# Kernel optimization log

Hardware: AMD Instinct MI355X
Metric: run time of the kernel (lower is better)

## Reference

```python
import jax, jax.numpy as jnp
import numpy as np

OVERSAMP = 2


def _pad_last2(x, H2, W2):
    # centered zero-pad of last two dims to (H2, W2) -- PadLast
    H, W = x.shape[-2], x.shape[-1]
    ph, pw = (H2 - H) // 2, (W2 - W) // 2
    pad = [(0, 0)] * (x.ndim - 2) + [(ph, H2 - H - ph), (pw, W2 - W - pw)]
    return jnp.pad(x, pad)


def _crop_last2(x, H, W):
    # centered crop of last two dims to (H, W) -- PadLast.adjoint
    H2, W2 = x.shape[-2], x.shape[-1]
    ph, pw = (H2 - H) // 2, (W2 - W) // 2
    return x[..., ph:ph + H, pw:pw + W]


def setup_inputs() -> dict:
    key = jax.random.key(0)
    ks = jax.random.split(key, 6)
    A, C, H, W = 5, 12, 256, 256
    Hp, Wp = OVERSAMP * H, OVERSAMP * W
    x_r = jax.random.normal(ks[0], (A, H, W), dtype=jnp.float32)
    x_i = jax.random.normal(ks[1], (A, H, W), dtype=jnp.float32)
    mps_r = jax.random.normal(ks[2], (C, H, W), dtype=jnp.float32) * 0.1
    mps_i = jax.random.normal(ks[3], (C, H, W), dtype=jnp.float32) * 0.1
    kern_r = jax.random.normal(ks[4], (A, A, Hp, Wp), dtype=jnp.float32) * 0.1
    kern_i = jax.random.normal(ks[5], (A, A, Hp, Wp), dtype=jnp.float32) * 0.1
    return {"x_r": x_r, "x_i": x_i, "mps_r": mps_r, "mps_i": mps_i,
            "kern_r": kern_r, "kern_i": kern_i}


def reference(x_r, x_i, mps_r, mps_i, kern_r, kern_i):
    # Toeplitz normal operator AHA_func: x [A,H,W] -> [A,H,W]
    x = jax.lax.complex(x_r, x_i)          # [A,H,W]
    mps = jax.lax.complex(mps_r, mps_i)    # [C,H,W]
    kernels = jax.lax.complex(kern_r, kern_i)  # [Aout,Ain,2H,2W]
    A, H, W = x.shape
    Hp, Wp = kernels.shape[-2], kernels.shape[-1]
    # coil modulation: x[None,:] * mps[:,None] -> [C,A,H,W]
    cx = mps[:, None, :, :] * x[None, :, :, :]
    cx = _pad_last2(cx, Hp, Wp)            # [C,A,2H,2W]
    Fx = jnp.fft.fftn(cx, axes=(-2, -1), norm='ortho')
    # Fx[:,None] [C,1,Ain,2H,2W] * kernels [Aout,Ain,2H,2W] -> [C,Aout,Ain,2H,2W]
    y = (OVERSAMP ** 2) * jnp.fft.ifftn(Fx[:, None, ...] * kernels,
                                        axes=(-2, -1), norm='ortho')
    y = jnp.sum(y, axis=2)                 # sum over Ain -> [C,Aout,2H,2W]
    y = _crop_last2(y, H, W)               # [C,A,H,W]
    y = y * jnp.conj(mps)[:, None, :, :]
    return jnp.sum(y, axis=0)              # [A,H,W]
```

## Files before the change

kernel.cpp:

```cpp
#include <hip/hip_runtime.h>
#include <cstddef>

#define PI_F 3.14159265358979323846f
#define A_  5
#define C_  12
#define RPG (C_ * A_)

__device__ float2 g_bufA[RPG * 256 * 512];
__device__ float2 g_bufB[RPG * 512 * 256];
__device__ float2 g_xT[5  * 65536];
__device__ float2 g_mT[12 * 65536];
__device__ float2 g_oT[5  * 65536];

#define NP 528
__device__ inline int PADI(int i) { return i + (i >> 5); }
__device__ inline int PADT(int i) { return i + (i >> 3); }

__device__ inline void build_tabP(float2* tab, int t) {
    #pragma unroll
    for (int q = 0; q < 2; ++q) {
        int k = t + q * 128;
        float s, c;
        __sincosf(-2.0f * PI_F * (float)k * (1.0f / 512.0f), &s, &c);
        tab[PADT(k)] = make_float2(c, s);
    }
}

template<int DIR>
__device__ inline float2 cmulw(float2 v, float2 w) {
    float cv = w.x, sv = (DIR < 0) ? w.y : -w.y;
    return make_float2(v.x * cv - v.y * sv, v.x * sv + v.y * cv);
}

template<int DIR>
__device__ void fft512(float* Ar, float* Ai, float* Br, float* Bi,
                       const float2* tab, int t) {
    float *srcR = Ar, *srcI = Ai, *dstR = Br, *dstI = Bi;
    int Ns = 1;
    #pragma unroll
    for (int s = 0; s < 4; ++s) {
        __syncthreads();
        int j = t;
        int m = j & (Ns - 1);
        int e1 = m << (7 - 2 * s);
        float2 w1 = tab[PADT(e1)], w2 = tab[PADT(2 * e1)];
        float2 w3 = make_float2(w1.x * w2.x - w1.y * w2.y,
                                w1.x * w2.y + w1.y * w2.x);
        int i0 = PADI(j), i1 = PADI(j + 128), i2 = PADI(j + 256), i3 = PADI(j + 384);
        float2 v0 = make_float2(srcR[i0], srcI[i0]);
        float2 v1 = cmulw<DIR>(make_float2(srcR[i1], srcI[i1]), w1);
        float2 v2 = cmulw<DIR>(make_float2(srcR[i2], srcI[i2]), w2);
        float2 v3 = cmulw<DIR>(make_float2(srcR[i3], srcI[i3]), w3);
        float2 t0 = make_float2(v0.x + v2.x, v0.y + v2.y);
        float2 t1 = make_float2(v0.x - v2.x, v0.y - v2.y);
        float2 t2 = make_float2(v1.x + v3.x, v1.y + v3.y);
        float2 t3 = make_float2(v1.x - v3.x, v1.y - v3.y);
        float2 y0 = make_float2(t0.x + t2.x, t0.y + t2.y);
        float2 y2 = make_float2(t0.x - t2.x, t0.y - t2.y);
        float2 y1, y3;
        if (DIR < 0) {
            y1 = make_float2(t1.x + t3.y, t1.y - t3.x);
            y3 = make_float2(t1.x - t3.y, t1.y + t3.x);
        } else {
            y1 = make_float2(t1.x - t3.y, t1.y + t3.x);
            y3 = make_float2(t1.x + t3.y, t1.y - t3.x);
        }
        int idxD = ((j & ~(Ns - 1)) << 2) | m;
        int o0 = PADI(idxD), o1 = PADI(idxD + Ns);
        int o2 = PADI(idxD + 2 * Ns), o3 = PADI(idxD + 3 * Ns);
        dstR[o0] = y0.x; dstI[o0] = y0.y;
        dstR[o1] = y1.x; dstI[o1] = y1.y;
        dstR[o2] = y2.x; dstI[o2] = y2.y;
        dstR[o3] = y3.x; dstI[o3] = y3.y;
        float* tr = srcR; srcR = dstR; dstR = tr;
        float* ti = srcI; srcI = dstI; dstI = ti;
        Ns <<= 2;
    }
    __syncthreads();
    #pragma unroll
    for (int q = 0; q < 2; ++q) {
        int j = t + q * 128;
        float2 w = tab[PADT(j)];
        int i0 = PADI(j), i1 = PADI(j + 256);
        float2 v0 = make_float2(srcR[i0], srcI[i0]);
        float2 tw = cmulw<DIR>(make_float2(srcR[i1], srcI[i1]), w);
        dstR[i0] = v0.x + tw.x; dstI[i0] = v0.y + tw.y;
        dstR[i1] = v0.x - tw.x; dstI[i1] = v0.y - tw.y;
    }
    __syncthreads();
}

__global__ void k_inT(const float* __restrict__ xr, const float* __restrict__ xi,
                      const float* __restrict__ mr, const float* __restrict__ mi) {
    __shared__ float tR[32][33], tI[32][33];
    int z = blockIdx.z;
    const float* pr; const float* pi; float2* dst;
    if (z < 5) {
        pr = xr + (size_t)z * 65536; pi = xi + (size_t)z * 65536;
        dst = g_xT + (size_t)z * 65536;
    } else {
        int c = z - 5;
        pr = mr + (size_t)c * 65536; pi = mi + (size_t)c * 65536;
        dst = g_mT + (size_t)c * 65536;
    }
    int w0 = blockIdx.x * 32, h0 = blockIdx.y * 32;
    int tx = threadIdx.x, ty = threadIdx.y;
    for (int i = ty; i < 32; i += 8) {
        size_t idx = (size_t)(h0 + i) * 256 + (w0 + tx);
        tR[i][tx] = pr[idx];
        tI[i][tx] = pi[idx];
    }
    __syncthreads();
    for (int i = ty; i < 32; i += 8)
        dst[(size_t)(w0 + i) * 256 + (h0 + tx)] =
            make_float2(tR[tx][i], tI[tx][i]);
}

__global__ void k_fft1c() {
    int row = blockIdx.x;
    int ca = row >> 8;
    int xcol = row & 255;
    int coil = ca / A_;
    int a = ca - coil * A_;
    int t = threadIdx.x;
    __shared__ float Are[NP], Aim[NP], Bre[NP], Bim[NP];
    __shared__ float2 tab[288];
    build_tabP(tab, t);
    const float2* xs = g_xT + (size_t)a * 65536 + (size_t)xcol * 256;
    const float2* ms = g_mT + (size_t)coil * 65536 + (size_t)xcol * 256;
    Are[PADI(t)] = 0.f;       Aim[PADI(t)] = 0.f;
    Are[PADI(t + 384)] = 0.f; Aim[PADI(t + 384)] = 0.f;
    {
        float2 xv = xs[t], mv = ms[t];
        int p = PADI(t + 128);
        Are[p] = xv.x * mv.x - xv.y * mv.y;
        Aim[p] = xv.x * mv.y + xv.y * mv.x;
        xv = xs[t + 128]; mv = ms[t + 128];
        p = PADI(t + 256);
        Are[p] = xv.x * mv.x - xv.y * mv.y;
        Aim[p] = xv.x * mv.y + xv.y * mv.x;
    }
    fft512<-1>(Are, Aim, Bre, Bim, tab, t);
    float2* o = (float2*)g_bufA + (size_t)row * 512;
    #pragma unroll
    for (int q = 0; q < 4; ++q) {
        int k = t + q * 128;
        int p = PADI(k);
        o[k] = make_float2(Bre[p], Bim[p]);
    }
}

__global__ void __launch_bounds__(128) k_colfmc(const float* __restrict__ kr,
                                                const float* __restrict__ ki) {
    int b = blockIdx.x;
    int xcd = b & 7;
    int s = b >> 3;
    int v = s / 96, w = s % 96;
    int u = xcd + (v << 3);
    int coil = w % C_;
    int ky = (u << 3) + (w / C_);
    int t = threadIdx.x;
    __shared__ float Sre[NP], Sim[NP];
    __shared__ float FR[A_][NP], FI[A_][NP];
    __shared__ float2 tab[288];
    build_tabP(tab, t);

    for (int ain = 0; ain < A_; ++ain) {
        const float2* src = (const float2*)g_bufA +
                            ((size_t)(coil * A_ + ain) << 17);
        float2 v1 = src[(size_t)t * 512 + ky];
        float2 v2 = src[(size_t)(t + 128) * 512 + ky];
        Sre[PADI(t)] = 0.f;       Sim[PADI(t)] = 0.f;
        Sre[PADI(t + 384)] = 0.f; Sim[PADI(t + 384)] = 0.f;
        int p = PADI(t + 128);
        Sre[p] = v1.x; Sim[p] = v1.y;
        p = PADI(t + 256);
        Sre[p] = v2.x; Sim[p] = v2.y;
        fft512<-1>(Sre, Sim, FR[ain], FI[ain], tab, t);
    }

    const float scale = 4.0f / 262144.0f;
    size_t kyBase = (size_t)ky << 9;
    #pragma unroll
    for (int q = 0; q < 4; ++q) {
        int kx = t + q * 128;
        float krB[25], kiB[25];
        #pragma unroll
        for (int m = 0; m < 25; ++m) {
            size_t idx = ((size_t)m << 18) + kyBase + kx;
            krB[m] = kr[idx];
            kiB[m] = ki[idx];
        }
        int p = PADI(kx);
        float fr[A_], fi[A_];
        #pragma unroll
        for (int ain = 0; ain < A_; ++ain) {
            fr[ain] = FR[ain][p];
            fi[ain] = FI[ain][p];
        }
        #pragma unroll
        for (int aout = 0; aout < A_; ++aout) {
            float gr = 0.f, gi = 0.f;
            #pragma unroll
            for (int ain = 0; ain < A_; ++ain) {
                float kre = krB[aout * A_ + ain], kim = kiB[aout * A_ + ain];
                gr += kre * fr[ain] - kim * fi[ain];
                gi += kre * fi[ain] + kim * fr[ain];
            }
            FR[aout][p] = scale * gr;
            FI[aout][p] = scale * gi;
        }
    }

    for (int aout = 0; aout < A_; ++aout) {
        fft512<1>(FR[aout], FI[aout], Sre, Sim, tab, t);
        float4* o4 = (float4*)((float2*)g_bufB +
            ((size_t)(coil * A_ + aout) * 512 + ky) * 256);
        int x0 = 128 + 2 * t;
        int p0 = PADI(x0), p1 = PADI(x0 + 1);
        o4[t] = make_float4(Sre[p0], Sim[p0], Sre[p1], Sim[p1]);
    }
}

__global__ void k_outfr() {
    int b = blockIdx.x;
    int xcd = b & 7;
    int s = b >> 3;
    int v = s >> 3, w = s & 7;
    int g = xcd + (v << 3);
    int a = g >> 5;
    int xcol = ((g & 31) << 3) + w;
    int t = threadIdx.x;
    __shared__ float Are[NP], Aim[NP], Bre[NP], Bim[NP];
    __shared__ float2 tab[288];
    build_tabP(tab, t);
    float ar0 = 0.f, ai0 = 0.f, ar1 = 0.f, ai1 = 0.f;
    int y0 = 128 + 2 * t;
    for (int c = 0; c < C_; ++c) {
        const float2* src = (const float2*)g_bufB +
                            ((size_t)(c * A_ + a) << 17);
        #pragma unroll
        for (int q = 0; q < 4; ++q) {
            int kyq = t + q * 128;
            float2 vv = src[(size_t)kyq * 256 + xcol];
            int p = PADI(kyq);
            Are[p] = vv.x; Aim[p] = vv.y;
        }
        fft512<1>(Are, Aim, Bre, Bim, tab, t);
        const float4* mp4 = (const float4*)(g_mT + (size_t)c * 65536 +
                                            (size_t)xcol * 256);
        float4 mm = mp4[t];
        int p0 = PADI(y0), p1 = PADI(y0 + 1);
        float v0x = Bre[p0], v0y = Bim[p0];
        float v1x = Bre[p1], v1y = Bim[p1];
        ar0 += v0x * mm.x + v0y * mm.y;  ai0 += v0y * mm.x - v0x * mm.y;
        ar1 += v1x * mm.z + v1y * mm.w;  ai1 += v1y * mm.z - v1x * mm.w;
    }
    float4* o4 = (float4*)(g_oT + (size_t)a * 65536 + (size_t)xcol * 256);
    o4[t] = make_float4(ar0, ai0, ar1, ai1);
}

__global__ void k_outT(float* __restrict__ out, int outFloats) {
    __shared__ float tR[32][33], tI[32][33];
    int a = blockIdx.z;
    int x0 = blockIdx.x * 32, y0 = blockIdx.y * 32;
    const float2* src = g_oT + (size_t)a * 65536;
    int tx = threadIdx.x, ty = threadIdx.y;
    for (int i = ty; i < 32; i += 8) {
        float2 vv = src[(size_t)(x0 + i) * 256 + (y0 + tx)];
        tR[i][tx] = vv.x; tI[i][tx] = vv.y;
    }
    __syncthreads();
    for (int i = ty; i < 32; i += 8) {
        size_t reIdx = (size_t)a * 65536 + (size_t)(y0 + i) * 256 + (x0 + tx);
        size_t imIdx = 327680 + reIdx;
        if (reIdx < (size_t)outFloats) out[reIdx] = tR[tx][i];
        if (imIdx < (size_t)outFloats) out[imIdx] = tI[tx][i];
    }
}

extern "C" void kernel_launch(void* const* d_in, const int* in_sizes, int n_in,
                              void* d_out, int out_size, void* d_ws, size_t ws_size,
                              hipStream_t stream) {
    const float* xr = (const float*)d_in[0];
    const float* xi = (const float*)d_in[1];
    const float* mr = (const float*)d_in[2];
    const float* mi = (const float*)d_in[3];
    const float* kr = (const float*)d_in[4];
    const float* ki = (const float*)d_in[5];
    float* out = (float*)d_out;
    (void)d_ws; (void)ws_size; (void)n_in; (void)in_sizes;

    k_inT   <<<dim3(8, 8, 17), dim3(32, 8), 0, stream>>>(xr, xi, mr, mi);
    k_fft1c <<<RPG * 256, 128, 0, stream>>>();
    k_colfmc<<<C_ * 512, 128, 0, stream>>>(kr, ki);
    k_outfr <<<A_ * 256, 128, 0, stream>>>();
    k_outT  <<<dim3(8, 8, 5), dim3(32, 8), 0, stream>>>(out, out_size);
}
```

Baseline: 312.6 us.

## Transpose intermediate buffer layouts, prefetch next slices, and fuse final output transpose

Both intermediate spectra buffers are re-laid out so the column-FFT kernel and the output kernel read contiguous float4 rows, while the producing kernels now do strided scatter writes. The final transpose kernel and its staging buffer are removed: k_outfr writes the cropped, coil-combined result directly into the output with strided stores. Software prefetching of the next input slice is added to the ain and coil loops, the LDS padding scheme becomes i+(i>>3), and the XCD-aware block remapping in k_outfr is dropped. The net effect depends on whether coalesced reads outweigh the newly uncoalesced writes.

```diff
diff --git a/kernel.cpp b/kernel.cpp
--- a/kernel.cpp
+++ b/kernel.cpp
@@ -6,23 +6,21 @@
 #define C_  12
 #define RPG (C_ * A_)
 
-__device__ float2 g_bufA[RPG * 256 * 512];
-__device__ float2 g_bufB[RPG * 512 * 256];
+__device__ float2 g_bufA[RPG * 512 * 256];
+__device__ float2 g_bufB[RPG * 256 * 512];
 __device__ float2 g_xT[5  * 65536];
 __device__ float2 g_mT[12 * 65536];
-__device__ float2 g_oT[5  * 65536];
-
-#define NP 528
-__device__ inline int PADI(int i) { return i + (i >> 5); }
-__device__ inline int PADT(int i) { return i + (i >> 3); }
-
-__device__ inline void build_tabP(float2* tab, int t) {
+
+#define NP 576
+__device__ inline int P(int i) { return i + (i >> 3); }
+
+__device__ inline void build_tab(float2* tab, int t) {
     #pragma unroll
     for (int q = 0; q < 2; ++q) {
         int k = t + q * 128;
         float s, c;
         __sincosf(-2.0f * PI_F * (float)k * (1.0f / 512.0f), &s, &c);
-        tab[PADT(k)] = make_float2(c, s);
+        tab[P(k)] = make_float2(c, s);
     }
 }
 
@@ -43,10 +41,10 @@
         int j = t;
         int m = j & (Ns - 1);
         int e1 = m << (7 - 2 * s);
-        float2 w1 = tab[PADT(e1)], w2 = tab[PADT(2 * e1)];
+        float2 w1 = tab[P(e1)], w2 = tab[P(2 * e1)];
         float2 w3 = make_float2(w1.x * w2.x - w1.y * w2.y,
                                 w1.x * w2.y + w1.y * w2.x);
-        int i0 = PADI(j), i1 = PADI(j + 128), i2 = PADI(j + 256), i3 = PADI(j + 384);
+        int i0 = P(j), i1 = P(j + 128), i2 = P(j + 256), i3 = P(j + 384);
         float2 v0 = make_float2(srcR[i0], srcI[i0]);
         float2 v1 = cmulw<DIR>(make_float2(srcR[i1], srcI[i1]), w1);
         float2 v2 = cmulw<DIR>(make_float2(srcR[i2], srcI[i2]), w2);
@@ -66,8 +64,8 @@
             y3 = make_float2(t1.x + t3.y, t1.y - t3.x);
         }
         int idxD = ((j & ~(Ns - 1)) << 2) | m;
-        int o0 = PADI(idxD), o1 = PADI(idxD + Ns);
-        int o2 = PADI(idxD + 2 * Ns), o3 = PADI(idxD + 3 * Ns);
+        int o0 = P(idxD), o1 = P(idxD + Ns);
+        int o2 = P(idxD + 2 * Ns), o3 = P(idxD + 3 * Ns);
         dstR[o0] = y0.x; dstI[o0] = y0.y;
         dstR[o1] = y1.x; dstI[o1] = y1.y;
         dstR[o2] = y2.x; dstI[o2] = y2.y;
@@ -80,8 +78,8 @@
     #pragma unroll
     for (int q = 0; q < 2; ++q) {
         int j = t + q * 128;
-        float2 w = tab[PADT(j)];
-        int i0 = PADI(j), i1 = PADI(j + 256);
+        float2 w = tab[P(j)];
+        int i0 = P(j), i1 = P(j + 256);
         float2 v0 = make_float2(srcR[i0], srcI[i0]);
         float2 tw = cmulw<DIR>(make_float2(srcR[i1], srcI[i1]), w);
         dstR[i0] = v0.x + tw.x; dstI[i0] = v0.y + tw.y;
@@ -125,28 +123,25 @@
     int t = threadIdx.x;
     __shared__ float Are[NP], Aim[NP], Bre[NP], Bim[NP];
     __shared__ float2 tab[288];
-    build_tabP(tab, t);
-    const float2* xs = g_xT + (size_t)a * 65536 + (size_t)xcol * 256;
-    const float2* ms = g_mT + (size_t)coil * 65536 + (size_t)xcol * 256;
-    Are[PADI(t)] = 0.f;       Aim[PADI(t)] = 0.f;
-    Are[PADI(t + 384)] = 0.f; Aim[PADI(t + 384)] = 0.f;
-    {
-        float2 xv = xs[t], mv = ms[t];
-        int p = PADI(t + 128);
-        Are[p] = xv.x * mv.x - xv.y * mv.y;
-        Aim[p] = xv.x * mv.y + xv.y * mv.x;
-        xv = xs[t + 128]; mv = ms[t + 128];
-        p = PADI(t + 256);
-        Are[p] = xv.x * mv.x - xv.y * mv.y;
-        Aim[p] = xv.x * mv.y + xv.y * mv.x;
-    }
+    build_tab(tab, t);
+    const float4* xs4 = (const float4*)(g_xT + (size_t)a * 65536 + (size_t)xcol * 256);
+    const float4* ms4 = (const float4*)(g_mT + (size_t)coil * 65536 + (size_t)xcol * 256);
+    float4 xv = xs4[t], mv = ms4[t];
+    Are[P(t)] = 0.f;       Aim[P(t)] = 0.f;
+    Are[P(t + 384)] = 0.f; Aim[P(t + 384)] = 0.f;
+    int p = P(128 + 2 * t);
+    Are[p] = xv.x * mv.x - xv.y * mv.y;
+    Aim[p] = xv.x * mv.y + xv.y * mv.x;
+    p = P(129 + 2 * t);
+    Are[p] = xv.z * mv.z - xv.w * mv.w;
+    Aim[p] = xv.z * mv.w + xv.w * mv.z;
     fft512<-1>(Are, Aim, Bre, Bim, tab, t);
-    float2* o = (float2*)g_bufA + (size_t)row * 512;
+    float2* o = g_bufA + (size_t)ca * 131072 + xcol;
     #pragma unroll
     for (int q = 0; q < 4; ++q) {
-        int k = t + q * 128;
-        int p = PADI(k);
-        o[k] = make_float2(Bre[p], Bim[p]);
+        int ky = t + q * 128;
+        int pp = P(ky);
+        o[(size_t)ky * 256] = make_float2(Bre[pp], Bim[pp]);
     }
 }
 
@@ -163,20 +158,22 @@
     __shared__ float Sre[NP], Sim[NP];
     __shared__ float FR[A_][NP], FI[A_][NP];
     __shared__ float2 tab[288];
-    build_tabP(tab, t);
-
+    build_tab(tab, t);
+
+    const float2* bA = g_bufA + ((size_t)coil * A_) * 131072 + (size_t)ky * 256;
+    float4 cur = ((const float4*)bA)[t];
     for (int ain = 0; ain < A_; ++ain) {
-        const float2* src = (const float2*)g_bufA +
-                            ((size_t)(coil * A_ + ain) << 17);
-        float2 v1 = src[(size_t)t * 512 + ky];
-        float2 v2 = src[(size_t)(t + 128) * 512 + ky];
-        Sre[PADI(t)] = 0.f;       Sim[PADI(t)] = 0.f;
-        Sre[PADI(t + 384)] = 0.f; Sim[PADI(t + 384)] = 0.f;
-        int p = PADI(t + 128);
-        Sre[p] = v1.x; Sim[p] = v1.y;
-        p = PADI(t + 256);
-        Sre[p] = v2.x; Sim[p] = v2.y;
+        float4 nxt = cur;
+        if (ain + 1 < A_)
+            nxt = ((const float4*)(bA + (size_t)(ain + 1) * 131072))[t];
+        Sre[P(t)] = 0.f;       Sim[P(t)] = 0.f;
+        Sre[P(t + 384)] = 0.f; Sim[P(t + 384)] = 0.f;
+        int p = P(128 + 2 * t);
+        Sre[p] = cur.x; Sim[p] = cur.y;
+        p = P(129 + 2 * t);
+        Sre[p] = cur.z; Sim[p] = cur.w;
         fft512<-1>(Sre, Sim, FR[ain], FI[ain], tab, t);
+        cur = nxt;
     }
 
     const float scale = 4.0f / 262144.0f;
@@ -191,7 +188,7 @@
             krB[m] = kr[idx];
             kiB[m] = ki[idx];
         }
-        int p = PADI(kx);
+        int p = P(kx);
         float fr[A_], fi[A_];
         #pragma unroll
         for (int ain = 0; ain < A_; ++ain) {
@@ -214,69 +211,54 @@
 
     for (int aout = 0; aout < A_; ++aout) {
         fft512<1>(FR[aout], FI[aout], Sre, Sim, tab, t);
-        float4* o4 = (float4*)((float2*)g_bufB +
-            ((size_t)(coil * A_ + aout) * 512 + ky) * 256);
-        int x0 = 128 + 2 * t;
-        int p0 = PADI(x0), p1 = PADI(x0 + 1);
-        o4[t] = make_float4(Sre[p0], Sim[p0], Sre[p1], Sim[p1]);
-    }
-}
-
-__global__ void k_outfr() {
+        float2* oB = g_bufB + ((size_t)(coil * A_ + aout)) * 131072 + ky;
+        int p0 = P(128 + 2 * t), p1 = P(129 + 2 * t);
+        oB[(size_t)(2 * t) * 512]     = make_float2(Sre[p0], Sim[p0]);
+        oB[(size_t)(2 * t + 1) * 512] = make_float2(Sre[p1], Sim[p1]);
+    }
+}
+
+__global__ void k_outfr(float* __restrict__ out, int outFloats) {
     int b = blockIdx.x;
-    int xcd = b & 7;
-    int s = b >> 3;
-    int v = s >> 3, w = s & 7;
-    int g = xcd + (v << 3);
-    int a = g >> 5;
-    int xcol = ((g & 31) << 3) + w;
+    int a = b >> 8;
+    int xcol = b & 255;
     int t = threadIdx.x;
     __shared__ float Are[NP], Aim[NP], Bre[NP], Bim[NP];
     __shared__ float2 tab[288];
-    build_tabP(tab, t);
+    build_tab(tab, t);
     float ar0 = 0.f, ai0 = 0.f, ar1 = 0.f, ai1 = 0.f;
-    int y0 = 128 + 2 * t;
+    const float2* bB = g_bufB + (size_t)a * 131072 + (size_t)xcol * 512;
+    const float2* mT = g_mT + (size_t)xcol * 256;
+    float4 c0 = ((const float4*)bB)[t];
+    float4 c1 = ((const float4*)bB)[t + 128];
+    float4 cm = ((const float4*)mT)[t];
     for (int c = 0; c < C_; ++c) {
-        const float2* src = (const float2*)g_bufB +
-                            ((size_t)(c * A_ + a) << 17);
-        #pragma unroll
-        for (int q = 0; q < 4; ++q) {
-            int kyq = t + q * 128;
-            float2 vv = src[(size_t)kyq * 256 + xcol];
-            int p = PADI(kyq);
-            Are[p] = vv.x; Aim[p] = vv.y;
+        int p = P(2 * t);       Are[p] = c0.x; Aim[p] = c0.y;
+        p = P(2 * t + 1);       Are[p] = c0.z; Aim[p] = c0.w;
+        p = P(256 + 2 * t);     Are[p] = c1.x; Aim[p] = c1.y;
+        p = P(257 + 2 * t);     Are[p] = c1.z; Aim[p] = c1.w;
+        float4 n0 = c0, n1 = c1, nm = cm;
+        if (c + 1 < C_) {
+            const float2* nB = bB + (size_t)(c + 1) * A_ * 131072;
+            n0 = ((const float4*)nB)[t];
+            n1 = ((const float4*)nB)[t + 128];
+            nm = ((const float4*)(mT + (size_t)(c + 1) * 65536))[t];
         }
         fft512<1>(Are, Aim, Bre, Bim, tab, t);
-        const float4* mp4 = (const float4*)(g_mT + (size_t)c * 65536 +
-                                            (size_t)xcol * 256);
-        float4 mm = mp4[t];
-        int p0 = PADI(y0), p1 = PADI(y0 + 1);
+        int p0 = P(128 + 2 * t), p1 = P(129 + 2 * t);
         float v0x = Bre[p0], v0y = Bim[p0];
         float v1x = Bre[p1], v1y = Bim[p1];
-        ar0 += v0x * mm.x + v0y * mm.y;  ai0 += v0y * mm.x - v0x * mm.y;
-        ar1 += v1x * mm.z + v1y * mm.w;  ai1 += v1y * mm.z - v1x * mm.w;
-    }
-    float4* o4 = (float4*)(g_oT + (size_t)a * 65536 + (size_t)xcol * 256);
-    o4[t] = make_float4(ar0, ai0, ar1, ai1);
-}
-
-__global__ void k_outT(float* __restrict__ out, int outFloats) {
-    __shared__ float tR[32][33], tI[32][33];
-    int a = blockIdx.z;
-    int x0 = blockIdx.x * 32, y0 = blockIdx.y * 32;
-    const float2* src = g_oT + (size_t)a * 65536;
-    int tx = threadIdx.x, ty = threadIdx.y;
-    for (int i = ty; i < 32; i += 8) {
-        float2 vv = src[(size_t)(x0 + i) * 256 + (y0 + tx)];
-        tR[i][tx] = vv.x; tI[i][tx] = vv.y;
-    }
-    __syncthreads();
-    for (int i = ty; i < 32; i += 8) {
-        size_t reIdx = (size_t)a * 65536 + (size_t)(y0 + i) * 256 + (x0 + tx);
-        size_t imIdx = 327680 + reIdx;
-        if (reIdx < (size_t)outFloats) out[reIdx] = tR[tx][i];
-        if (imIdx < (size_t)outFloats) out[imIdx] = tI[tx][i];
-    }
+        ar0 += v0x * cm.x + v0y * cm.y;  ai0 += v0y * cm.x - v0x * cm.y;
+        ar1 += v1x * cm.z + v1y * cm.w;  ai1 += v1y * cm.z - v1x * cm.w;
+        c0 = n0; c1 = n1; cm = nm;
+    }
+    size_t r0 = (size_t)a * 65536 + (size_t)(2 * t) * 256 + xcol;
+    size_t r1 = r0 + 256;
+    size_t i0 = 327680 + r0, i1 = 327680 + r1;
+    if (r0 < (size_t)outFloats) out[r0] = ar0;
+    if (r1 < (size_t)outFloats) out[r1] = ar1;
+    if (i0 < (size_t)outFloats) out[i0] = ai0;
+    if (i1 < (size_t)outFloats) out[i1] = ai1;
 }
 
 extern "C" void kernel_launch(void* const* d_in, const int* in_sizes, int n_in,
@@ -294,6 +276,5 @@
     k_inT   <<<dim3(8, 8, 17), dim3(32, 8), 0, stream>>>(xr, xi, mr, mi);
     k_fft1c <<<RPG * 256, 128, 0, stream>>>();
     k_colfmc<<<C_ * 512, 128, 0, stream>>>(kr, ki);
-    k_outfr <<<A_ * 256, 128, 0, stream>>>();
-    k_outT  <<<dim3(8, 8, 5), dim3(32, 8), 0, stream>>>(out, out_size);
-}
+    k_outfr <<<A_ * 256, 128, 0, stream>>>(out, out_size);
+}
```

After: 396.2 us. +26.7%, slower.
